# Optimization experiments

Measured on AMD Instinct MI355X. Metric: run time of the kernel, lower is better.

The kernel has to match this reference:

```python
import jax, jax.numpy as jnp
import numpy as np

NHID = 1024
NOUT = 50257
NLAY = 1
MAX_LEN = 24


def setup_inputs() -> dict:
    key = jax.random.key(0)
    ks = jax.random.split(key, 16)
    s = 0.02
    return {
        "inp": jax.random.randint(ks[0], (1,), 0, NOUT),
        "hidden": jax.random.normal(ks[1], (1, 1, NHID), dtype=jnp.float32),
        "encoder_output": jax.random.normal(ks[2], (1, NHID), dtype=jnp.float32),
        "encoder_outputs": jax.random.normal(ks[3], (MAX_LEN, NHID), dtype=jnp.float32),
        "emb_W": jax.random.normal(ks[4], (NOUT, NHID), dtype=jnp.float32) * s,
        "attn_W": jax.random.normal(ks[5], (MAX_LEN, 2 * NHID), dtype=jnp.float32) * s,
        "attn_b": jnp.zeros((MAX_LEN,), dtype=jnp.float32),
        "comb_W": jax.random.normal(ks[6], (NHID, 2 * NHID), dtype=jnp.float32) * s,
        "comb_b": jnp.zeros((NHID,), dtype=jnp.float32),
        "W_ih": jax.random.normal(ks[7], (3 * NHID, NHID), dtype=jnp.float32) * s,
        "W_hh": jax.random.normal(ks[8], (3 * NHID, NHID), dtype=jnp.float32) * s,
        "b_ih": jnp.zeros((3 * NHID,), dtype=jnp.float32),
        "b_hh": jnp.zeros((3 * NHID,), dtype=jnp.float32),
        "out_W": jax.random.normal(ks[9], (NOUT, NHID), dtype=jnp.float32) * s,
        "out_b": jnp.zeros((NOUT,), dtype=jnp.float32),
    }


def reference(inp, hidden, encoder_output, encoder_outputs, emb_W, attn_W, attn_b,
              comb_W, comb_b, W_ih, W_hh, b_ih, b_hh, out_W, out_b):
    # embedding lookup (dropout is identity in eval); [1, nhid]
    embedded = emb_W[inp]
    h = hidden[0]  # [1, nhid]
    # Bahdanau-style attention over encoder_outputs [max_len, nhid]
    attn_in = jnp.concatenate([embedded, h], axis=1)            # [1, 2*nhid]
    attn_weights = jax.nn.softmax(attn_in @ attn_W.T + attn_b, axis=-1)  # [1, max_len]
    attn_applied = attn_weights @ encoder_outputs               # [1, nhid]
    out = jnp.concatenate([embedded, attn_applied], axis=1) @ comb_W.T + comb_b  # [1, nhid]
    # nlay repeated (relu -> GRU step) with the same single-layer GRU weights
    for _ in range(NLAY):
        x = jax.nn.relu(out)
        gi = x @ W_ih.T + b_ih   # [1, 3*nhid]
        gh = h @ W_hh.T + b_hh   # [1, 3*nhid]
        ir, iz, i_n = jnp.split(gi, 3, axis=1)
        hr, hz, h_n = jnp.split(gh, 3, axis=1)
        r = jax.nn.sigmoid(ir + hr)
        z = jax.nn.sigmoid(iz + hz)
        n = jnp.tanh(i_n + r * h_n)
        h = (1.0 - z) * n + z * h
        out = h
    logp = jax.nn.log_softmax(out @ out_W.T + out_b, axis=-1)   # [1, nout]
    return (logp, h[None, :, :], attn_weights)
```

## Files before the change

### kernel.cpp

```cpp
#include <hip/hip_runtime.h>
#include <math.h>

#define NHID 1024
#define NOUT 50257
#define MAXLEN 24

#define WS_APP   0
#define WS_OUT   1024
#define WS_H     2048
#define WS_LOGIT 4096
#define WS_PAIRS 56320

__device__ __forceinline__ float wave_reduce_sum(float v) {
    #pragma unroll
    for (int off = 32; off > 0; off >>= 1) v += __shfl_down(v, off, 64);
    return v;
}

__device__ __forceinline__ void lse_merge(float& m, float& s, float m2, float s2) {
    float M = fmaxf(m, m2);
    s = s * expf(m - M) + s2 * expf(m2 - M);
    m = M;
}

__global__ void k_attn(const int* __restrict__ inp, const float* __restrict__ hid,
                       const float* __restrict__ enc, const float* __restrict__ embW,
                       const float* __restrict__ attnW, const float* __restrict__ attnb,
                       float* __restrict__ ws, float* __restrict__ out) {
    __shared__ float s_sc[MAXLEN];
    __shared__ float s_w[MAXLEN];
    const int tid = threadIdx.x;
    const int lane = tid & 63, wave = tid >> 6;
    const float4* emb4 = (const float4*)(embW + (size_t)inp[0] * NHID);
    const float4* hid4 = (const float4*)hid;
    for (int i = wave; i < MAXLEN; i += 4) {
        const float4* w4 = (const float4*)(attnW + (size_t)i * 2 * NHID);
        float acc = 0.f;
        #pragma unroll
        for (int it = 0; it < 8; ++it) {
            int idx = it * 64 + lane;
            float4 w = w4[idx];
            float4 a = (idx < 256) ? emb4[idx] : hid4[idx - 256];
            acc += w.x * a.x + w.y * a.y + w.z * a.z + w.w * a.w;
        }
        acc = wave_reduce_sum(acc);
        if (lane == 0) s_sc[i] = acc + attnb[i];
    }
    __syncthreads();
    if (tid == 0) {
        float m = -1e30f;
        for (int i = 0; i < MAXLEN; ++i) m = fmaxf(m, s_sc[i]);
        float s = 0.f;
        for (int i = 0; i < MAXLEN; ++i) { float e = expf(s_sc[i] - m); s_w[i] = e; s += e; }
        float inv = 1.f / s;
        for (int i = 0; i < MAXLEN; ++i) { s_w[i] *= inv; out[NOUT + NHID + i] = s_w[i]; }
    }
    __syncthreads();
    for (int j = tid; j < NHID; j += 256) {
        float acc = 0.f;
        #pragma unroll 4
        for (int i = 0; i < MAXLEN; ++i) acc += s_w[i] * enc[i * NHID + j];
        ws[WS_APP + j] = acc;
    }
}

__global__ void k_comb(const int* __restrict__ inp, const float* __restrict__ embW,
                       const float* __restrict__ combW, const float* __restrict__ combb,
                       float* __restrict__ ws) {
    const int j = blockIdx.x, t = threadIdx.x;
    const float4* emb4 = (const float4*)(embW + (size_t)inp[0] * NHID);
    const float4* app4 = (const float4*)(ws + WS_APP);
    const float4* w4 = (const float4*)(combW + (size_t)j * 2 * NHID);
    float4 wa = w4[t],       xa = emb4[t];
    float4 wb = w4[256 + t], xb = app4[t];
    float p = wa.x * xa.x + wa.y * xa.y + wa.z * xa.z + wa.w * xa.w
            + wb.x * xb.x + wb.y * xb.y + wb.z * xb.z + wb.w * xb.w;
    p = wave_reduce_sum(p);
    __shared__ float s_r[4];
    if ((t & 63) == 0) s_r[t >> 6] = p;
    __syncthreads();
    if (t == 0) ws[WS_OUT + j] = s_r[0] + s_r[1] + s_r[2] + s_r[3] + combb[j];
}

__global__ void k_gru(const float* __restrict__ hid, const float* __restrict__ Wih,
                      const float* __restrict__ Whh, const float* __restrict__ bih,
                      const float* __restrict__ bhh, float* __restrict__ ws,
                      float* __restrict__ out) {
    const int j = blockIdx.x, t = threadIdx.x;
    const float4* x4 = (const float4*)(ws + WS_OUT);
    const float4* h4 = (const float4*)hid;
    float4 xv = x4[t];
    xv.x = fmaxf(xv.x, 0.f); xv.y = fmaxf(xv.y, 0.f);
    xv.z = fmaxf(xv.z, 0.f); xv.w = fmaxf(xv.w, 0.f);
    float4 hv = h4[t];
    float p[6];
    #pragma unroll
    for (int r = 0; r < 3; ++r) {
        float4 wv = ((const float4*)(Wih + (size_t)(r * NHID + j) * NHID))[t];
        p[r] = wv.x * xv.x + wv.y * xv.y + wv.z * xv.z + wv.w * xv.w;
    }
    #pragma unroll
    for (int r = 0; r < 3; ++r) {
        float4 wv = ((const float4*)(Whh + (size_t)(r * NHID + j) * NHID))[t];
        p[3 + r] = wv.x * hv.x + wv.y * hv.y + wv.z * hv.z + wv.w * hv.w;
    }
    __shared__ float s_r[6][4];
    #pragma unroll
    for (int r = 0; r < 6; ++r) {
        float v = wave_reduce_sum(p[r]);
        if ((t & 63) == 0) s_r[r][t >> 6] = v;
    }
    __syncthreads();
    if (t == 0) {
        float g[6];
        #pragma unroll
        for (int r = 0; r < 6; ++r) g[r] = s_r[r][0] + s_r[r][1] + s_r[r][2] + s_r[r][3];
        float ir = g[0] + bih[j],            hr = g[3] + bhh[j];
        float iz = g[1] + bih[NHID + j],     hz = g[4] + bhh[NHID + j];
        float in_ = g[2] + bih[2 * NHID + j], hn = g[5] + bhh[2 * NHID + j];
        float r_ = 1.f / (1.f + expf(-(ir + hr)));
        float z_ = 1.f / (1.f + expf(-(iz + hz)));
        float n_ = tanhf(in_ + r_ * hn);
        float hnew = (1.f - z_) * n_ + z_ * hid[j];
        ws[WS_H + j] = hnew;
        out[NOUT + j] = hnew;
    }
}

__global__ void k_logits(const float* __restrict__ outW, const float* __restrict__ outb,
                         float* __restrict__ ws) {
    const int lane = threadIdx.x & 63, wave = threadIdx.x >> 6;
    const int row = blockIdx.x * 4 + wave;
    if (row >= NOUT) return;
    const float4* w4 = (const float4*)(outW + (size_t)row * NHID);
    const float4* h4 = (const float4*)(ws + WS_H);
    float acc = 0.f;
    #pragma unroll
    for (int it = 0; it < 4; ++it) {
        int idx = it * 64 + lane;
        float4 w = w4[idx], h = h4[idx];
        acc += w.x * h.x + w.y * h.y + w.z * h.z + w.w * h.w;
    }
    acc = wave_reduce_sum(acc);
    if (lane == 0) ws[WS_LOGIT + row] = acc + outb[row];
}

__global__ void k_lse_partial(const float* __restrict__ logits, float* __restrict__ pairs) {
    const int tid = threadIdx.x;
    const int i = blockIdx.x * 256 + tid;
    float m = -1e30f, s = 0.f;
    if (i < NOUT) { m = logits[i]; s = 1.f; }
    #pragma unroll
    for (int off = 32; off > 0; off >>= 1) {
        float m2 = __shfl_down(m, off, 64);
        float s2 = __shfl_down(s, off, 64);
        lse_merge(m, s, m2, s2);
    }
    __shared__ float sm[4], ss[4];
    if ((tid & 63) == 0) { sm[tid >> 6] = m; ss[tid >> 6] = s; }
    __syncthreads();
    if (tid == 0) {
        float M = sm[0], S = ss[0];
        lse_merge(M, S, sm[1], ss[1]);
        lse_merge(M, S, sm[2], ss[2]);
        lse_merge(M, S, sm[3], ss[3]);
        pairs[2 * blockIdx.x] = M;
        pairs[2 * blockIdx.x + 1] = S;
    }
}

__global__ void k_finalize(const float* __restrict__ logits, const float* __restrict__ pairs,
                           float* __restrict__ out) {
    const int tid = threadIdx.x;
    float m = pairs[2 * tid], s = pairs[2 * tid + 1];
    #pragma unroll
    for (int off = 32; off > 0; off >>= 1) {
        float m2 = __shfl_down(m, off, 64);
        float s2 = __shfl_down(s, off, 64);
        lse_merge(m, s, m2, s2);
    }
    __shared__ float sm[4], ss[4];
    __shared__ float sC;
    if ((tid & 63) == 0) { sm[tid >> 6] = m; ss[tid >> 6] = s; }
    __syncthreads();
    if (tid == 0) {
        float M = sm[0], S = ss[0];
        lse_merge(M, S, sm[1], ss[1]);
        lse_merge(M, S, sm[2], ss[2]);
        lse_merge(M, S, sm[3], ss[3]);
        sC = M + logf(S);
    }
    __syncthreads();
    const float C = sC;
    const int i = blockIdx.x * 256 + tid;
    if (i < NOUT) out[i] = logits[i] - C;
}

extern "C" void kernel_launch(void* const* d_in, const int* in_sizes, int n_in,
                              void* d_out, int out_size, void* d_ws, size_t ws_size,
                              hipStream_t stream) {
    const int*   inp   = (const int*)d_in[0];
    const float* hid   = (const float*)d_in[1];
    const float* enc   = (const float*)d_in[3];
    const float* embW  = (const float*)d_in[4];
    const float* attnW = (const float*)d_in[5];
    const float* attnb = (const float*)d_in[6];
    const float* combW = (const float*)d_in[7];
    const float* combb = (const float*)d_in[8];
    const float* Wih   = (const float*)d_in[9];
    const float* Whh   = (const float*)d_in[10];
    const float* bih   = (const float*)d_in[11];
    const float* bhh   = (const float*)d_in[12];
    const float* outW  = (const float*)d_in[13];
    const float* outb  = (const float*)d_in[14];
    float* out = (float*)d_out;
    float* ws  = (float*)d_ws;

    hipLaunchKernelGGL(k_attn, dim3(1), dim3(256), 0, stream,
                       inp, hid, enc, embW, attnW, attnb, ws, out);
    hipLaunchKernelGGL(k_comb, dim3(NHID), dim3(256), 0, stream,
                       inp, embW, combW, combb, ws);
    hipLaunchKernelGGL(k_gru, dim3(NHID), dim3(256), 0, stream,
                       hid, Wih, Whh, bih, bhh, ws, out);
    hipLaunchKernelGGL(k_logits, dim3((NOUT + 3) / 4), dim3(256), 0, stream,
                       outW, outb, ws);
    hipLaunchKernelGGL(k_lse_partial, dim3(256), dim3(256), 0, stream,
                       ws + WS_LOGIT, ws + WS_PAIRS);
    hipLaunchKernelGGL(k_finalize, dim3(256), dim3(256), 0, stream,
                       ws + WS_LOGIT, ws + WS_PAIRS, out);
}
```

Measured before the change: 437.2 us.

## Overlap W_hh GEMV with attention and fuse LSE partials into logits kernel

Moves the hidden-state GEMV (W_hh·h) out of the GRU kernel into extra blocks of the attention launch, so it runs alongside the single-block attention. The GRU kernel then reads the precomputed gates. The logits kernel is restructured to compute 64 rows per 1024-thread block and emit per-block log-sum-exp partials, which removes the separate partial-reduction launch. ReLU is folded into the combine kernel's output. Together these cut one launch and move work off the serialized GRU step, at the cost of a larger first kernel and different block shapes.

Measured after the change: 426.5 us. 2.5% less time.

```diff
diff --git a/kernel.cpp b/kernel.cpp
--- a/kernel.cpp
+++ b/kernel.cpp
@@ -6,10 +6,13 @@
 #define MAXLEN 24
 
 #define WS_APP   0
-#define WS_OUT   1024
-#define WS_H     2048
-#define WS_LOGIT 4096
-#define WS_PAIRS 56320
+#define WS_X     1024
+#define WS_GH    2048
+#define WS_H     5120
+#define WS_LOGIT 8192
+#define WS_PAIRS 61440
+
+#define LOG_BLOCKS 786
 
 __device__ __forceinline__ float wave_reduce_sum(float v) {
     #pragma unroll
@@ -23,17 +26,35 @@
     m = M;
 }
 
-__global__ void k_attn(const int* __restrict__ inp, const float* __restrict__ hid,
-                       const float* __restrict__ enc, const float* __restrict__ embW,
-                       const float* __restrict__ attnW, const float* __restrict__ attnb,
-                       float* __restrict__ ws, float* __restrict__ out) {
+__global__ __launch_bounds__(1024) void
+k_attn_gh(const int* __restrict__ inp, const float* __restrict__ hid,
+          const float* __restrict__ enc, const float* __restrict__ embW,
+          const float* __restrict__ attnW, const float* __restrict__ attnb,
+          const float* __restrict__ Whh, const float* __restrict__ bhh,
+          float* __restrict__ ws, float* __restrict__ out) {
+    const int tid = threadIdx.x;
+    const int lane = tid & 63, wave = tid >> 6;
+    const float4* hid4 = (const float4*)hid;
+
+    if (blockIdx.x > 0) {
+        const int row = (blockIdx.x - 1) * 16 + wave;
+        const float4* w4 = (const float4*)(Whh + (size_t)row * NHID);
+        float acc = 0.f;
+        #pragma unroll
+        for (int it = 0; it < 4; ++it) {
+            int idx = it * 64 + lane;
+            float4 w = w4[idx], h = hid4[idx];
+            acc += w.x * h.x + w.y * h.y + w.z * h.z + w.w * h.w;
+        }
+        acc = wave_reduce_sum(acc);
+        if (lane == 0) ws[WS_GH + row] = acc + bhh[row];
+        return;
+    }
+
     __shared__ float s_sc[MAXLEN];
     __shared__ float s_w[MAXLEN];
-    const int tid = threadIdx.x;
-    const int lane = tid & 63, wave = tid >> 6;
     const float4* emb4 = (const float4*)(embW + (size_t)inp[0] * NHID);
-    const float4* hid4 = (const float4*)hid;
-    for (int i = wave; i < MAXLEN; i += 4) {
+    for (int i = wave; i < MAXLEN; i += 16) {
         const float4* w4 = (const float4*)(attnW + (size_t)i * 2 * NHID);
         float acc = 0.f;
         #pragma unroll
@@ -56,17 +77,18 @@
         for (int i = 0; i < MAXLEN; ++i) { s_w[i] *= inv; out[NOUT + NHID + i] = s_w[i]; }
     }
     __syncthreads();
-    for (int j = tid; j < NHID; j += 256) {
+    {
         float acc = 0.f;
         #pragma unroll 4
-        for (int i = 0; i < MAXLEN; ++i) acc += s_w[i] * enc[i * NHID + j];
-        ws[WS_APP + j] = acc;
-    }
-}
-
-__global__ void k_comb(const int* __restrict__ inp, const float* __restrict__ embW,
-                       const float* __restrict__ combW, const float* __restrict__ combb,
-                       float* __restrict__ ws) {
+        for (int i = 0; i < MAXLEN; ++i) acc += s_w[i] * enc[i * NHID + tid];
+        ws[WS_APP + tid] = acc;
+    }
+}
+
+__global__ __launch_bounds__(256) void
+k_comb(const int* __restrict__ inp, const float* __restrict__ embW,
+       const float* __restrict__ combW, const float* __restrict__ combb,
+       float* __restrict__ ws) {
     const int j = blockIdx.x, t = threadIdx.x;
     const float4* emb4 = (const float4*)(embW + (size_t)inp[0] * NHID);
     const float4* app4 = (const float4*)(ws + WS_APP);
@@ -79,121 +101,110 @@
     __shared__ float s_r[4];
     if ((t & 63) == 0) s_r[t >> 6] = p;
     __syncthreads();
-    if (t == 0) ws[WS_OUT + j] = s_r[0] + s_r[1] + s_r[2] + s_r[3] + combb[j];
-}
-
-__global__ void k_gru(const float* __restrict__ hid, const float* __restrict__ Wih,
-                      const float* __restrict__ Whh, const float* __restrict__ bih,
-                      const float* __restrict__ bhh, float* __restrict__ ws,
-                      float* __restrict__ out) {
+    if (t == 0) ws[WS_X + j] = fmaxf(s_r[0] + s_r[1] + s_r[2] + s_r[3] + combb[j], 0.f);
+}
+
+__global__ __launch_bounds__(256) void
+k_gru(const float* __restrict__ hid, const float* __restrict__ Wih,
+      const float* __restrict__ bih, float* __restrict__ ws,
+      float* __restrict__ out) {
     const int j = blockIdx.x, t = threadIdx.x;
-    const float4* x4 = (const float4*)(ws + WS_OUT);
-    const float4* h4 = (const float4*)hid;
+    const float4* x4 = (const float4*)(ws + WS_X);
     float4 xv = x4[t];
-    xv.x = fmaxf(xv.x, 0.f); xv.y = fmaxf(xv.y, 0.f);
-    xv.z = fmaxf(xv.z, 0.f); xv.w = fmaxf(xv.w, 0.f);
-    float4 hv = h4[t];
-    float p[6];
+    float p[3];
     #pragma unroll
     for (int r = 0; r < 3; ++r) {
         float4 wv = ((const float4*)(Wih + (size_t)(r * NHID + j) * NHID))[t];
         p[r] = wv.x * xv.x + wv.y * xv.y + wv.z * xv.z + wv.w * xv.w;
     }
+    __shared__ float s_r[3][4];
     #pragma unroll
     for (int r = 0; r < 3; ++r) {
-        float4 wv = ((const float4*)(Whh + (size_t)(r * NHID + j) * NHID))[t];
-        p[3 + r] = wv.x * hv.x + wv.y * hv.y + wv.z * hv.z + wv.w * hv.w;
-    }
-    __shared__ float s_r[6][4];
-    #pragma unroll
-    for (int r = 0; r < 6; ++r) {
         float v = wave_reduce_sum(p[r]);
         if ((t & 63) == 0) s_r[r][t >> 6] = v;
     }
     __syncthreads();
     if (t == 0) {
-        float g[6];
-        #pragma unroll
-        for (int r = 0; r < 6; ++r) g[r] = s_r[r][0] + s_r[r][1] + s_r[r][2] + s_r[r][3];
-        float ir = g[0] + bih[j],            hr = g[3] + bhh[j];
-        float iz = g[1] + bih[NHID + j],     hz = g[4] + bhh[NHID + j];
-        float in_ = g[2] + bih[2 * NHID + j], hn = g[5] + bhh[2 * NHID + j];
-        float r_ = 1.f / (1.f + expf(-(ir + hr)));
-        float z_ = 1.f / (1.f + expf(-(iz + hz)));
-        float n_ = tanhf(in_ + r_ * hn);
+        float gi[3];
+        #pragma unroll
+        for (int r = 0; r < 3; ++r) gi[r] = s_r[r][0] + s_r[r][1] + s_r[r][2] + s_r[r][3] + bih[r * NHID + j];
+        float hr = ws[WS_GH + j], hz = ws[WS_GH + NHID + j], hn = ws[WS_GH + 2 * NHID + j];
+        float r_ = 1.f / (1.f + expf(-(gi[0] + hr)));
+        float z_ = 1.f / (1.f + expf(-(gi[1] + hz)));
+        float n_ = tanhf(gi[2] + r_ * hn);
         float hnew = (1.f - z_) * n_ + z_ * hid[j];
         ws[WS_H + j] = hnew;
         out[NOUT + j] = hnew;
     }
 }
 
-__global__ void k_logits(const float* __restrict__ outW, const float* __restrict__ outb,
-                         float* __restrict__ ws) {
-    const int lane = threadIdx.x & 63, wave = threadIdx.x >> 6;
-    const int row = blockIdx.x * 4 + wave;
-    if (row >= NOUT) return;
-    const float4* w4 = (const float4*)(outW + (size_t)row * NHID);
+__global__ __launch_bounds__(1024) void
+k_logits(const float* __restrict__ outW, const float* __restrict__ outb,
+         float* __restrict__ ws) {
+    const int tid = threadIdx.x;
+    const int lane = tid & 63, wave = tid >> 6;
     const float4* h4 = (const float4*)(ws + WS_H);
-    float acc = 0.f;
-    #pragma unroll
-    for (int it = 0; it < 4; ++it) {
-        int idx = it * 64 + lane;
-        float4 w = w4[idx], h = h4[idx];
-        acc += w.x * h.x + w.y * h.y + w.z * h.z + w.w * h.w;
-    }
-    acc = wave_reduce_sum(acc);
-    if (lane == 0) ws[WS_LOGIT + row] = acc + outb[row];
-}
-
-__global__ void k_lse_partial(const float* __restrict__ logits, float* __restrict__ pairs) {
+    float4 hv[4];
+    #pragma unroll
+    for (int it = 0; it < 4; ++it) hv[it] = h4[it * 64 + lane];
+    float m = -1e30f, s = 0.f;
+    const int rowBase = blockIdx.x * 64 + wave * 4;
+    #pragma unroll
+    for (int rr = 0; rr < 4; ++rr) {
+        const int row = rowBase + rr;
+        if (row >= NOUT) break;
+        const float4* w4 = (const float4*)(outW + (size_t)row * NHID);
+        float acc = 0.f;
+        #pragma unroll
+        for (int it = 0; it < 4; ++it) {
+            float4 w = w4[it * 64 + lane];
+            acc += w.x * hv[it].x + w.y * hv[it].y + w.z * hv[it].z + w.w * hv[it].w;
+        }
+        acc = wave_reduce_sum(acc);
+        if (lane == 0) {
+            float v = acc + outb[row];
+            ws[WS_LOGIT + row] = v;
+            lse_merge(m, s, v, 1.f);
+        }
+    }
+    __shared__ float sm[16], ss[16];
+    if (lane == 0) { sm[wave] = m; ss[wave] = s; }
+    __syncthreads();
+    if (tid == 0) {
+        float M = sm[0], S = ss[0];
+        #pragma unroll
+        for (int w = 1; w < 16; ++w) lse_merge(M, S, sm[w], ss[w]);
+        ws[WS_PAIRS + 2 * blockIdx.x] = M;
+        ws[WS_PAIRS + 2 * blockIdx.x + 1] = S;
+    }
+}
+
+__global__ __launch_bounds__(1024) void
+k_finalize(const float* __restrict__ ws, float* __restrict__ out) {
     const int tid = threadIdx.x;
-    const int i = blockIdx.x * 256 + tid;
+    const int lane = tid & 63, wave = tid >> 6;
     float m = -1e30f, s = 0.f;
-    if (i < NOUT) { m = logits[i]; s = 1.f; }
+    if (tid < LOG_BLOCKS) { m = ws[WS_PAIRS + 2 * tid]; s = ws[WS_PAIRS + 2 * tid + 1]; }
     #pragma unroll
     for (int off = 32; off > 0; off >>= 1) {
         float m2 = __shfl_down(m, off, 64);
         float s2 = __shfl_down(s, off, 64);
         lse_merge(m, s, m2, s2);
     }
-    __shared__ float sm[4], ss[4];
-    if ((tid & 63) == 0) { sm[tid >> 6] = m; ss[tid >> 6] = s; }
+    __shared__ float sm[16], ss[16];
+    __shared__ float sC;
+    if (lane == 0) { sm[wave] = m; ss[wave] = s; }
     __syncthreads();
     if (tid == 0) {
         float M = sm[0], S = ss[0];
-        lse_merge(M, S, sm[1], ss[1]);
-        lse_merge(M, S, sm[2], ss[2]);
-        lse_merge(M, S, sm[3], ss[3]);
-        pairs[2 * blockIdx.x] = M;
-        pairs[2 * blockIdx.x + 1] = S;
-    }
-}
-
-__global__ void k_finalize(const float* __restrict__ logits, const float* __restrict__ pairs,
-                           float* __restrict__ out) {
-    const int tid = threadIdx.x;
-    float m = pairs[2 * tid], s = pairs[2 * tid + 1];
-    #pragma unroll
-    for (int off = 32; off > 0; off >>= 1) {
-        float m2 = __shfl_down(m, off, 64);
-        float s2 = __shfl_down(s, off, 64);
-        lse_merge(m, s, m2, s2);
-    }
-    __shared__ float sm[4], ss[4];
-    __shared__ float sC;
-    if ((tid & 63) == 0) { sm[tid >> 6] = m; ss[tid >> 6] = s; }
-    __syncthreads();
-    if (tid == 0) {
-        float M = sm[0], S = ss[0];
-        lse_merge(M, S, sm[1], ss[1]);
-        lse_merge(M, S, sm[2], ss[2]);
-        lse_merge(M, S, sm[3], ss[3]);
+        #pragma unroll
+        for (int w = 1; w < 16; ++w) lse_merge(M, S, sm[w], ss[w]);
         sC = M + logf(S);
     }
     __syncthreads();
     const float C = sC;
-    const int i = blockIdx.x * 256 + tid;
-    if (i < NOUT) out[i] = logits[i] - C;
+    const int i = blockIdx.x * 1024 + tid;
+    if (i < NOUT) out[i] = ws[WS_LOGIT + i] - C;
 }
 
 extern "C" void kernel_launch(void* const* d_in, const int* in_sizes, int n_in,
@@ -216,16 +227,14 @@
     float* out = (float*)d_out;
     float* ws  = (float*)d_ws;
 
-    hipLaunchKernelGGL(k_attn, dim3(1), dim3(256), 0, stream,
-                       inp, hid, enc, embW, attnW, attnb, ws, out);
+    hipLaunchKernelGGL(k_attn_gh, dim3(1 + 192), dim3(1024), 0, stream,
+                       inp, hid, enc, embW, attnW, attnb, Whh, bhh, ws, out);
     hipLaunchKernelGGL(k_comb, dim3(NHID), dim3(256), 0, stream,
                        inp, embW, combW, combb, ws);
     hipLaunchKernelGGL(k_gru, dim3(NHID), dim3(256), 0, stream,
-                       hid, Wih, Whh, bih, bhh, ws, out);
-    hipLaunchKernelGGL(k_logits, dim3((NOUT + 3) / 4), dim3(256), 0, stream,
+                       hid, Wih, bih, ws, out);
+    hipLaunchKernelGGL(k_logits, dim3(LOG_BLOCKS), dim3(1024), 0, stream,
                        outW, outb, ws);
-    hipLaunchKernelGGL(k_lse_partial, dim3(256), dim3(256), 0, stream,
-                       ws + WS_LOGIT, ws + WS_PAIRS);
-    hipLaunchKernelGGL(k_finalize, dim3(256), dim3(256), 0, stream,
-                       ws + WS_LOGIT, ws + WS_PAIRS, out);
-}
+    hipLaunchKernelGGL(k_finalize, dim3(50), dim3(1024), 0, stream,
+                       ws, out);
+}
```
